# Performance work log

Measured on AMD Instinct MI355X. Metric: run time of the kernel, lower is better.

## Reference

```python
import jax, jax.numpy as jnp
import numpy as np

# TT factorization for fc1: 768 = 4*4*6*8 -> 3072 = 4*6*8*16, ranks (1,12,24,12,1)
# TT factorization for fc2: 3072 = 4*6*8*16 -> 768 = 4*4*6*8, ranks (1,12,24,12,1)
IN_F1, OUT_F1 = (4, 4, 6, 8), (4, 6, 8, 16)
IN_F2, OUT_F2 = (4, 6, 8, 16), (4, 4, 6, 8)
RANKS = (12, 24, 12)


def _core(key, shape, fan_in):
    return jax.random.normal(key, shape, dtype=jnp.float32) * (fan_in ** -0.5)


def make_tt_params(key, in_f, out_f, ranks):
    r = (1,) + tuple(ranks) + (1,)
    ks = jax.random.split(key, 5)
    # boundary cores squeeze the unit rank dims
    g1 = _core(ks[0], (in_f[0], out_f[0], r[1]), in_f[0])              # (i1,o1,r1)
    g2 = _core(ks[1], (r[1], in_f[1], out_f[1], r[2]), r[1] * in_f[1])  # (r1,i2,o2,r2)
    g3 = _core(ks[2], (r[2], in_f[2], out_f[2], r[3]), r[2] * in_f[2])  # (r2,i3,o3,r3)
    g4 = _core(ks[3], (r[3], in_f[3], out_f[3]), r[3] * in_f[3])        # (r3,i4,o4)
    b = jnp.zeros((int(np.prod(out_f)),), dtype=jnp.float32)
    return g1, g2, g3, g4, b


def tt_linear(x2d, g1, g2, g3, g4, bias, in_f):
    # x2d: (N, prod(in_f)) -> (N, prod(out_f))
    z = x2d.reshape((-1,) + tuple(in_f))                  # (b,i1,i2,i3,i4)
    z = jnp.einsum('bijkl,ipr->bjklpr', z, g1)            # (b,i2,i3,i4,o1,r1)
    z = jnp.einsum('bjklpr,rjqs->bklpqs', z, g2)          # (b,i3,i4,o1,o2,r2)
    z = jnp.einsum('bklpqs,sktu->blpqtu', z, g3)          # (b,i4,o1,o2,o3,r3)
    z = jnp.einsum('blpqtu,ulv->bpqtv', z, g4)            # (b,o1,o2,o3,o4)
    return z.reshape(z.shape[0], -1) + bias


def setup_inputs() -> dict:
    key = jax.random.key(0)
    kx, k1, k2 = jax.random.split(key, 3)
    x = jax.random.normal(kx, (2, 2048, 768), dtype=jnp.float32)
    g1a, g1b, g1c, g1d, b1 = make_tt_params(k1, IN_F1, OUT_F1, RANKS)
    g2a, g2b, g2c, g2d, b2 = make_tt_params(k2, IN_F2, OUT_F2, RANKS)
    return {"x": x, "g1a": g1a, "g1b": g1b, "g1c": g1c, "g1d": g1d, "b1": b1,
            "g2a": g2a, "g2b": g2b, "g2c": g2c, "g2d": g2d, "b2": b2}


def reference(x, g1a, g1b, g1c, g1d, b1, g2a, g2b, g2c, g2d, b2):
    B, S, D = x.shape
    h = tt_linear(x.reshape(-1, D), g1a, g1b, g1c, g1d, b1, IN_F1)  # (N, 3072)
    h = jax.nn.gelu(h, approximate=False)  # nn.GELU() default = exact erf
    # dropout: identity in eval mode
    y = tt_linear(h, g2a, g2b, g2c, g2d, b2, IN_F2)                 # (N, 768)
    return y.reshape(B, S, -1)
```

## Files before the change

kernel.cpp:

```cpp
#include <hip/hip_runtime.h>
#include <cstdint>
#include <cstddef>

typedef unsigned short u16;
typedef __attribute__((ext_vector_type(8))) __bf16 bf16x8;
typedef __attribute__((ext_vector_type(4))) float f32x4;

__device__ __forceinline__ u16 f2bf(float f) {
  unsigned u = __float_as_uint(f);
  u += 0x7FFFu + ((u >> 16) & 1u);
  return (u16)(u >> 16);
}

__device__ __forceinline__ float bf2f(u16 h) {
  return __uint_as_float(((unsigned)h) << 16);
}

__device__ __forceinline__ void async16(u16* lds, const u16* g) {
  __builtin_amdgcn_global_load_lds(
      (const __attribute__((address_space(1))) unsigned int*)g,
      (__attribute__((address_space(3))) unsigned int*)lds, 16, 0, 0);
}

__global__ __launch_bounds__(256)
void prep(const float4* __restrict__ x4, ushort4* __restrict__ xb4,
          const float* __restrict__ gA1, const float* __restrict__ gB1,
          const float* __restrict__ gC1, const float* __restrict__ gD1,
          const float* __restrict__ gA2, const float* __restrict__ gB2,
          const float* __restrict__ gC2, const float* __restrict__ gD2,
          float* __restrict__ B12_1, float* __restrict__ B12_2,
          float* __restrict__ C1, float* __restrict__ C2) {
  const int b = blockIdx.x;
  const int tid = threadIdx.x;
  if (b < 3072) {
    int i = b * 256 + tid;
    float4 v = x4[i];
    ushort4 o;
    o.x = f2bf(v.x); o.y = f2bf(v.y); o.z = f2bf(v.z); o.w = f2bf(v.w);
    xb4[i] = o;
    return;
  }
  int idx = (b - 3072) * 256 + tid;
  if (idx < 9216) {
    int e = idx;
    int r2 = e % 24; int t = e / 24;
    int fo12 = t % 24, fi12 = t / 24;
    int i2 = fi12 % 4, i1 = fi12 / 4;
    int o2 = fo12 % 6, o1 = fo12 / 6;
    float s = 0.f;
#pragma unroll
    for (int r1 = 0; r1 < 12; ++r1)
      s += gA1[(i1 * 4 + o1) * 12 + r1] * gB1[((r1 * 4 + i2) * 6 + o2) * 24 + r2];
    B12_1[e] = s;
  } else if (idx < 18432) {
    int e = idx - 9216;
    int r2 = e % 24; int t = e / 24;
    int fo12 = t % 16, fi12 = t / 16;
    int i2 = fi12 % 6, i1 = fi12 / 6;
    int o2 = fo12 % 4, o1 = fo12 / 4;
    float s = 0.f;
#pragma unroll
    for (int r1 = 0; r1 < 12; ++r1)
      s += gA2[(i1 * 4 + o1) * 12 + r1] * gB2[((r1 * 6 + i2) * 4 + o2) * 24 + r2];
    B12_2[e] = s;
  } else if (idx < 165888) {
    int e = idx - 18432;
    int fi34 = e % 48; int t = e / 48;
    int fo34 = t % 128;
    int i3 = fi34 / 8, i4 = fi34 % 8;
    int o3 = fo34 / 16, o4 = fo34 % 16;
    int r2 = t / 128;
    float s = 0.f;
#pragma unroll
    for (int r3 = 0; r3 < 12; ++r3)
      s += gC1[((r2 * 6 + i3) * 8 + o3) * 12 + r3] * gD1[(r3 * 8 + i4) * 16 + o4];
    C1[e] = s;
  } else {
    int e = idx - 165888;
    int fi34 = e % 128; int t = e / 128;
    int fo34 = t % 48;
    int i3 = fi34 / 16, i4 = fi34 % 16;
    int o3 = fo34 / 8, o4 = fo34 % 8;
    int r2 = t / 48;
    float s = 0.f;
#pragma unroll
    for (int r3 = 0; r3 < 12; ++r3)
      s += gC2[((r2 * 8 + i3) * 6 + o3) * 12 + r3] * gD2[(r3 * 16 + i4) * 8 + o4];
    C2[e] = s;
  }
}

template <int FI12, int I34, int O12, int O34, int OG>
__device__ __forceinline__
void tt_expand_body(const float* __restrict__ B12, const float* __restrict__ C34t,
                    u16* __restrict__ Wt, int bx, int by, int tid, float* sB) {
  constexpr int R2 = 24;
  constexpr int Kin = FI12 * I34;
  constexpr int IC = Kin / 8;
  constexpr int I34C = I34 / 8;
  for (int e = tid; e < FI12 * OG * R2; e += 256) {
    int r2 = e % R2; int t = e / R2;
    int f = t % OG; int fi12 = t / OG;
    sB[(fi12 * OG + f) * 25 + r2] = B12[(fi12 * O12 + by * OG + f) * R2 + r2];
  }
  __syncthreads();
  const int t = bx * 256 + tid;
  const int fo34 = t / IC;
  const int ic = t % IC;
  const int fi12 = ic / I34C;
  const int fi34 = (ic % I34C) * 8;

  float acc[OG][8];
#pragma unroll
  for (int f = 0; f < OG; ++f)
#pragma unroll
    for (int k = 0; k < 8; ++k) acc[f][k] = 0.f;

  for (int r2 = 0; r2 < R2; ++r2) {
    const float4* cp = (const float4*)(C34t + ((size_t)(r2 * O34 + fo34) * I34 + fi34));
    float4 c0 = cp[0], c1 = cp[1];
    float c[8] = {c0.x, c0.y, c0.z, c0.w, c1.x, c1.y, c1.z, c1.w};
#pragma unroll
    for (int f = 0; f < OG; ++f) {
      float bb = sB[(fi12 * OG + f) * 25 + r2];
#pragma unroll
      for (int k = 0; k < 8; ++k) acc[f][k] += bb * c[k];
    }
  }
#pragma unroll
  for (int f = 0; f < OG; ++f) {
    int out = (by * OG + f) * O34 + fo34;
    u16 v[8];
#pragma unroll
    for (int k = 0; k < 8; ++k) v[k] = f2bf(acc[f][k]);
    *(uint4*)(Wt + (size_t)out * Kin + fi12 * I34 + fi34) = *(const uint4*)v;
  }
}

__global__ __launch_bounds__(256)
void tt_expand2(const float* __restrict__ B12_1, const float* __restrict__ C1, u16* __restrict__ W1t,
                const float* __restrict__ B12_2, const float* __restrict__ C2, u16* __restrict__ W2t) {
  __shared__ float sB[24 * 4 * 25];
  const int b = blockIdx.x;
  const int tid = threadIdx.x;
  if (b < 288) {
    tt_expand_body<16, 48, 24, 128, 4>(B12_1, C1, W1t, b % 48, b / 48, tid, sB);
  } else {
    int bb = b - 288;
    tt_expand_body<24, 128, 16, 48, 4>(B12_2, C2, W2t, bb % 72, bb / 72, tid, sB);
  }
}

__global__ void reduceN8(const uint4* __restrict__ P, const float* __restrict__ bias,
                         float4* __restrict__ out4, int n8, int zstride8, int nz) {
  int i = blockIdx.x * 256 + threadIdx.x;
  if (i >= n8) return;
  int b0 = (i % 96) * 8;
  float a[8];
#pragma unroll
  for (int k = 0; k < 8; ++k) a[k] = bias[b0 + k];
  for (int s = 0; s < nz; ++s) {
    uint4 u = P[i + s * zstride8];
    const u16* up = (const u16*)&u;
#pragma unroll
    for (int k = 0; k < 8; ++k) a[k] += bf2f(up[k]);
  }
  out4[i * 2]     = (float4){a[0], a[1], a[2], a[3]};
  out4[i * 2 + 1] = (float4){a[4], a[5], a[6], a[7]};
}

template <bool GELU, int MAP>
__global__ __launch_bounds__(512, 2)
void gemm_bt(const u16* __restrict__ A, const u16* __restrict__ Bt,
             const float* __restrict__ bias, u16* __restrict__ Out,
             int N, int lda, int ldb, size_t zstride) {
  constexpr int NT = 12;
  const int flat = blockIdx.x;
  const int xcd = flat & 7;
  const int local = flat >> 3;
  int bm, bn, bz;
  if (MAP == 1) {
    bm = (xcd >> 1) * 4 + (local & 3);
    bn = (xcd & 1) * 8 + (local >> 2);
    bz = 0;
  } else {
    bz = xcd >> 1;
    bm = (xcd & 1) * 8 + (local & 7);
    bn = local >> 3;
  }
  const int kbeg = (MAP == 2) ? bz * 768 : 0;

  __shared__ __align__(16) u16 AL[2][16384];
  __shared__ __align__(16) u16 BL[3][12288];

  const int tid = threadIdx.x;
  const int wave = tid >> 6, lane = tid & 63;
  const int lr = lane & 15, lq = lane >> 4;
  const int wr = (wave >> 2) * 128;
  const int wc = (wave & 3) * 48;

  const int prow = tid >> 3;
  const int pcc  = (tid & 7) ^ (((tid >> 5) & 1) << 1);
  const u16* Ag = A + (size_t)(bm * 256 + prow) * lda + kbeg + pcc * 8;
  const u16* Bg = Bt + (size_t)(bn * 192 + prow) * ldb + kbeg + pcc * 8;

  auto stA = [&](int slot, int p, int k) {
    async16(&AL[slot][0] + p * 4096 + tid * 8, Ag + (size_t)(p * 64) * lda + k);
  };
  auto stB = [&](int slot, int p, int k) {
    async16(&BL[slot][0] + p * 4096 + tid * 8, Bg + (size_t)(p * 64) * ldb + k);
  };

  int aOff[2][8], bOff[2][3];
#pragma unroll
  for (int kk = 0; kk < 2; ++kk) {
#pragma unroll
    for (int mi = 0; mi < 8; ++mi) {
      int L = (wr + mi * 16 + lr) * 128 + kk * 64 + lq * 16;
      L ^= ((L >> 9) & 1) << 5;
      aOff[kk][mi] = L >> 1;
    }
#pragma unroll
    for (int nj = 0; nj < 3; ++nj) {
      int L = (wc + nj * 16 + lr) * 128 + kk * 64 + lq * 16;
      L ^= ((L >> 9) & 1) << 5;
      bOff[kk][nj] = L >> 1;
    }
  }

  f32x4 acc[8][3];
#pragma unroll
  for (int mi = 0; mi < 8; ++mi)
#pragma unroll
    for (int nj = 0; nj < 3; ++nj) acc[mi][nj] = (f32x4){0.f, 0.f, 0.f, 0.f};

  stA(0, 0, 0); stA(0, 1, 0); stA(0, 2, 0); stA(0, 3, 0);
  stB(0, 0, 0); stB(0, 1, 0); stB(0, 2, 0);
  stB(1, 0, 64); stB(1, 1, 64); stB(1, 2, 64);
  asm volatile("s_waitcnt vmcnt(3)" ::: "memory");
  __builtin_amdgcn_s_barrier();
  __builtin_amdgcn_sched_barrier(0);

  int bsR = 0, bsW = 2;
  for (int t = 0; t < NT; ++t) {
    const u16* Ab = &AL[t & 1][0];
    const u16* Bb = &BL[bsR][0];
    const int wAs = (t + 1) & 1;
    const int kA = ((t + 1 < NT) ? t + 1 : NT - 1) * 64;
    const int kB = ((t + 2 < NT) ? t + 2 : NT - 1) * 64;

    bf16x8 bf[3], af[4], af2[4];
#pragma unroll
    for (int nj = 0; nj < 3; ++nj) bf[nj] = *(const bf16x8*)(Bb + bOff[0][nj]);
#pragma unroll
    for (int mi = 0; mi < 4; ++mi) af[mi] = *(const bf16x8*)(Ab + aOff[0][mi]);
    stA(wAs, 0, kA); stA(wAs, 1, kA);
    __builtin_amdgcn_s_barrier();
    asm volatile("s_waitcnt lgkmcnt(0)" ::: "memory");
    __builtin_amdgcn_sched_barrier(0);
    __builtin_amdgcn_s_setprio(1);
#pragma unroll
    for (int mi = 0; mi < 4; ++mi)
#pragma unroll
      for (int nj = 0; nj < 3; ++nj)
        acc[mi][nj] = __builtin_amdgcn_mfma_f32_16x16x32_bf16(af[mi], bf[nj], acc[mi][nj], 0, 0, 0);
    __builtin_amdgcn_s_setprio(0);
    __builtin_amdgcn_s_barrier();
    __builtin_amdgcn_sched_barrier(0);
#pragma unroll
    for (int mi = 0; mi < 4; ++mi) af2[mi] = *(const bf16x8*)(Ab + aOff[0][4 + mi]);
    stA(wAs, 2, kA); stA(wAs, 3, kA);
    __builtin_amdgcn_s_barrier();
    asm volatile("s_waitcnt lgkmcnt(0)" ::: "memory");
    __builtin_amdgcn_sched_barrier(0);
    __builtin_amdgcn_s_setprio(1);
#pragma unroll
    for (int mi = 0; mi < 4; ++mi)
#pragma unroll
      for (int nj = 0; nj < 3; ++nj)
        acc[4 + mi][nj] = __builtin_amdgcn_mfma_f32_16x16x32_bf16(af2[mi], bf[nj], acc[4 + mi][nj], 0, 0, 0);
    __builtin_amdgcn_s_setprio(0);
    __builtin_amdgcn_s_barrier();
    __builtin_amdgcn_sched_barrier(0);
#pragma unroll
    for (int nj = 0; nj < 3; ++nj) bf[nj] = *(const bf16x8*)(Bb + bOff[1][nj]);
#pragma unroll
    for (int mi = 0; mi < 4; ++mi) af[mi] = *(const bf16x8*)(Ab + aOff[1][mi]);
    stB(bsW, 0, kB); stB(bsW, 1, kB);
    __builtin_amdgcn_s_barrier();
    asm volatile("s_waitcnt lgkmcnt(0)" ::: "memory");
    __builtin_amdgcn_sched_barrier(0);
    __builtin_amdgcn_s_setprio(1);
#pragma unroll
    for (int mi = 0; mi < 4; ++mi)
#pragma unroll
      for (int nj = 0; nj < 3; ++nj)
        acc[mi][nj] = __builtin_amdgcn_mfma_f32_16x16x32_bf16(af[mi], bf[nj], acc[mi][nj], 0, 0, 0);
    __builtin_amdgcn_s_setprio(0);
    __builtin_amdgcn_s_barrier();
    __builtin_amdgcn_sched_barrier(0);
#pragma unroll
    for (int mi = 0; mi < 4; ++mi) af2[mi] = *(const bf16x8*)(Ab + aOff[1][4 + mi]);
    stB(bsW, 2, kB);
    __builtin_amdgcn_s_barrier();
    asm volatile("s_waitcnt lgkmcnt(0)" ::: "memory");
    __builtin_amdgcn_sched_barrier(0);
    __builtin_amdgcn_s_setprio(1);
#pragma unroll
    for (int mi = 0; mi < 4; ++mi)
#pragma unroll
      for (int nj = 0; nj < 3; ++nj)
        acc[4 + mi][nj] = __builtin_amdgcn_mfma_f32_16x16x32_bf16(af2[mi], bf[nj], acc[4 + mi][nj], 0, 0, 0);
    __builtin_amdgcn_s_setprio(0);
    asm volatile("s_waitcnt vmcnt(3)" ::: "memory");
    __builtin_amdgcn_s_barrier();
    __builtin_amdgcn_sched_barrier(0);

    bsR = (bsR + 1 == 3) ? 0 : bsR + 1;
    bsW = (bsW + 1 == 3) ? 0 : bsW + 1;
  }

  u16* Op = Out + (size_t)bz * zstride;
  const int r0 = bm * 256 + wr + lq * 4;
  const int c0 = bn * 192 + wc + lr;
  float bv[3];
  if (GELU) {
#pragma unroll
    for (int nj = 0; nj < 3; ++nj) bv[nj] = bias[c0 + nj * 16];
  }
#pragma unroll
  for (int mi = 0; mi < 8; ++mi) {
#pragma unroll
    for (int r = 0; r < 4; ++r) {
      const size_t rowoff = (size_t)(r0 + mi * 16 + r) * N;
#pragma unroll
      for (int nj = 0; nj < 3; ++nj) {
        float v = acc[mi][nj][r];
        if (GELU) {
          v += bv[nj];
          float inner = v * fmaf(v * v, 0.0356774081f, 0.7978845608f);
          float e = __builtin_amdgcn_exp2f(2.8853900818f * inner);
          float r1 = __builtin_amdgcn_rcpf(1.0f + e);
          v = v - v * r1;
        }
        Op[rowoff + c0 + nj * 16] = f2bf(v);
      }
    }
  }
}

extern "C" void kernel_launch(void* const* d_in, const int* in_sizes, int n_in,
                              void* d_out, int out_size, void* d_ws, size_t ws_size,
                              hipStream_t stream) {
  const float* x   = (const float*)d_in[0];
  const float* g1a = (const float*)d_in[1];
  const float* g1b = (const float*)d_in[2];
  const float* g1c = (const float*)d_in[3];
  const float* g1d = (const float*)d_in[4];
  const float* b1  = (const float*)d_in[5];
  const float* g2a = (const float*)d_in[6];
  const float* g2b = (const float*)d_in[7];
  const float* g2c = (const float*)d_in[8];
  const float* g2d = (const float*)d_in[9];
  const float* b2  = (const float*)d_in[10];
  float* out = (float*)d_out;

  char* ws = (char*)d_ws;
  u16* xb   = (u16*)(ws + 0);
  u16* W1t  = (u16*)(ws + 6291456);
  u16* W2t  = (u16*)(ws + 11010048);
  u16* h    = (u16*)(ws + 15728640);
  u16* Part = (u16*)(ws + 40894464);
  float* B12_1 = (float*)(ws + 40894464);
  float* B12_2 = (float*)(ws + 40894464 + 36864);
  float* C1    = (float*)(ws + 40894464 + 73728);
  float* C2    = (float*)(ws + 40894464 + 663552);

  prep<<<4296, 256, 0, stream>>>((const float4*)x, (ushort4*)xb,
                                 g1a, g1b, g1c, g1d, g2a, g2b, g2c, g2d,
                                 B12_1, B12_2, C1, C2);

  tt_expand2<<<576, 256, 0, stream>>>(B12_1, C1, W1t, B12_2, C2, W2t);

  gemm_bt<true, 1><<<256, 512, 0, stream>>>(xb, W1t, b1, h, 3072, 768, 768, 0);
  gemm_bt<false, 2><<<256, 512, 0, stream>>>(h, W2t, nullptr, Part, 768, 3072, 3072, 3145728);
  reduceN8<<<1536, 256, 0, stream>>>((const uint4*)Part, b2,
                                     (float4*)out, 393216, 393216, 4);
}
```

Measured before the change: 160.1 us.

## Shrink GEMM tiles to 128x96 with 4 waves and halve split-K

Reworks the bf16 GEMM kernel to use 128x96 output tiles with 256 threads (4 waves, each 64x48) in place of 256x192 tiles with 512 threads. This quadruples the block count for fc1 and doubles it for fc2, so the per-iteration pipeline drops from four MFMA phases to two. For fc2 the split-K factor goes from 4 to 2 with 24 K-steps per block, which halves the partial buffers the reduction reads. The aim is better occupancy and less partial-sum traffic, at the cost of lower operand reuse per tile and more global and LDS traffic per FLOP.

```diff
diff --git a/kernel.cpp b/kernel.cpp
--- a/kernel.cpp
+++ b/kernel.cpp
@@ -169,68 +169,67 @@
   out4[i * 2 + 1] = (float4){a[4], a[5], a[6], a[7]};
 }
 
-template <bool GELU, int MAP>
-__global__ __launch_bounds__(512, 2)
+template <bool GELU, int MAP, int NT>
+__global__ __launch_bounds__(256, 2)
 void gemm_bt(const u16* __restrict__ A, const u16* __restrict__ Bt,
              const float* __restrict__ bias, u16* __restrict__ Out,
              int N, int lda, int ldb, size_t zstride) {
-  constexpr int NT = 12;
   const int flat = blockIdx.x;
   const int xcd = flat & 7;
   const int local = flat >> 3;
   int bm, bn, bz;
   if (MAP == 1) {
-    bm = (xcd >> 1) * 4 + (local & 3);
-    bn = (xcd & 1) * 8 + (local >> 2);
+    bm = (xcd >> 1) * 8 + (local & 7);
+    bn = (xcd & 1) * 16 + (local >> 3);
     bz = 0;
   } else {
-    bz = xcd >> 1;
-    bm = (xcd & 1) * 8 + (local & 7);
+    bz = xcd & 1;
+    bm = (xcd >> 1) * 8 + (local & 7);
     bn = local >> 3;
   }
-  const int kbeg = (MAP == 2) ? bz * 768 : 0;
-
-  __shared__ __align__(16) u16 AL[2][16384];
-  __shared__ __align__(16) u16 BL[3][12288];
+  const int kbeg = (MAP == 2) ? bz * 1536 : 0;
+
+  __shared__ __align__(16) u16 AL[2][8192];
+  __shared__ __align__(16) u16 BL[3][6144];
 
   const int tid = threadIdx.x;
   const int wave = tid >> 6, lane = tid & 63;
   const int lr = lane & 15, lq = lane >> 4;
-  const int wr = (wave >> 2) * 128;
-  const int wc = (wave & 3) * 48;
+  const int wm = (wave & 1) * 64;
+  const int wn = (wave >> 1) * 48;
 
   const int prow = tid >> 3;
   const int pcc  = (tid & 7) ^ (((tid >> 5) & 1) << 1);
-  const u16* Ag = A + (size_t)(bm * 256 + prow) * lda + kbeg + pcc * 8;
-  const u16* Bg = Bt + (size_t)(bn * 192 + prow) * ldb + kbeg + pcc * 8;
+  const u16* Ag = A + (size_t)(bm * 128 + prow) * lda + kbeg + pcc * 8;
+  const u16* Bg = Bt + (size_t)(bn * 96 + prow) * ldb + kbeg + pcc * 8;
 
   auto stA = [&](int slot, int p, int k) {
-    async16(&AL[slot][0] + p * 4096 + tid * 8, Ag + (size_t)(p * 64) * lda + k);
+    async16(&AL[slot][0] + p * 2048 + tid * 8, Ag + (size_t)(p * 32) * lda + k);
   };
   auto stB = [&](int slot, int p, int k) {
-    async16(&BL[slot][0] + p * 4096 + tid * 8, Bg + (size_t)(p * 64) * ldb + k);
+    async16(&BL[slot][0] + p * 2048 + tid * 8, Bg + (size_t)(p * 32) * ldb + k);
   };
 
-  int aOff[2][8], bOff[2][3];
+  int aOff[2][4], bOff[2][3];
 #pragma unroll
   for (int kk = 0; kk < 2; ++kk) {
 #pragma unroll
-    for (int mi = 0; mi < 8; ++mi) {
-      int L = (wr + mi * 16 + lr) * 128 + kk * 64 + lq * 16;
+    for (int mi = 0; mi < 4; ++mi) {
+      int L = (wm + mi * 16 + lr) * 128 + kk * 64 + lq * 16;
       L ^= ((L >> 9) & 1) << 5;
       aOff[kk][mi] = L >> 1;
     }
 #pragma unroll
     for (int nj = 0; nj < 3; ++nj) {
-      int L = (wc + nj * 16 + lr) * 128 + kk * 64 + lq * 16;
+      int L = (wn + nj * 16 + lr) * 128 + kk * 64 + lq * 16;
       L ^= ((L >> 9) & 1) << 5;
       bOff[kk][nj] = L >> 1;
     }
   }
 
-  f32x4 acc[8][3];
-#pragma unroll
-  for (int mi = 0; mi < 8; ++mi)
+  f32x4 acc[4][3];
+#pragma unroll
+  for (int mi = 0; mi < 4; ++mi)
 #pragma unroll
     for (int nj = 0; nj < 3; ++nj) acc[mi][nj] = (f32x4){0.f, 0.f, 0.f, 0.f};
 
@@ -249,12 +248,12 @@
     const int kA = ((t + 1 < NT) ? t + 1 : NT - 1) * 64;
     const int kB = ((t + 2 < NT) ? t + 2 : NT - 1) * 64;
 
-    bf16x8 bf[3], af[4], af2[4];
+    bf16x8 bf[3], af[4];
 #pragma unroll
     for (int nj = 0; nj < 3; ++nj) bf[nj] = *(const bf16x8*)(Bb + bOff[0][nj]);
 #pragma unroll
     for (int mi = 0; mi < 4; ++mi) af[mi] = *(const bf16x8*)(Ab + aOff[0][mi]);
-    stA(wAs, 0, kA); stA(wAs, 1, kA);
+    stA(wAs, 0, kA); stA(wAs, 1, kA); stA(wAs, 2, kA); stA(wAs, 3, kA);
     __builtin_amdgcn_s_barrier();
     asm volatile("s_waitcnt lgkmcnt(0)" ::: "memory");
     __builtin_amdgcn_sched_barrier(0);
@@ -268,8 +267,10 @@
     __builtin_amdgcn_s_barrier();
     __builtin_amdgcn_sched_barrier(0);
 #pragma unroll
-    for (int mi = 0; mi < 4; ++mi) af2[mi] = *(const bf16x8*)(Ab + aOff[0][4 + mi]);
-    stA(wAs, 2, kA); stA(wAs, 3, kA);
+    for (int nj = 0; nj < 3; ++nj) bf[nj] = *(const bf16x8*)(Bb + bOff[1][nj]);
+#pragma unroll
+    for (int mi = 0; mi < 4; ++mi) af[mi] = *(const bf16x8*)(Ab + aOff[1][mi]);
+    stB(bsW, 0, kB); stB(bsW, 1, kB); stB(bsW, 2, kB);
     __builtin_amdgcn_s_barrier();
     asm volatile("s_waitcnt lgkmcnt(0)" ::: "memory");
     __builtin_amdgcn_sched_barrier(0);
@@ -278,39 +279,7 @@
     for (int mi = 0; mi < 4; ++mi)
 #pragma unroll
       for (int nj = 0; nj < 3; ++nj)
-        acc[4 + mi][nj] = __builtin_amdgcn_mfma_f32_16x16x32_bf16(af2[mi], bf[nj], acc[4 + mi][nj], 0, 0, 0);
-    __builtin_amdgcn_s_setprio(0);
-    __builtin_amdgcn_s_barrier();
-    __builtin_amdgcn_sched_barrier(0);
-#pragma unroll
-    for (int nj = 0; nj < 3; ++nj) bf[nj] = *(const bf16x8*)(Bb + bOff[1][nj]);
-#pragma unroll
-    for (int mi = 0; mi < 4; ++mi) af[mi] = *(const bf16x8*)(Ab + aOff[1][mi]);
-    stB(bsW, 0, kB); stB(bsW, 1, kB);
-    __builtin_amdgcn_s_barrier();
-    asm volatile("s_waitcnt lgkmcnt(0)" ::: "memory");
-    __builtin_amdgcn_sched_barrier(0);
-    __builtin_amdgcn_s_setprio(1);
-#pragma unroll
-    for (int mi = 0; mi < 4; ++mi)
-#pragma unroll
-      for (int nj = 0; nj < 3; ++nj)
         acc[mi][nj] = __builtin_amdgcn_mfma_f32_16x16x32_bf16(af[mi], bf[nj], acc[mi][nj], 0, 0, 0);
-    __builtin_amdgcn_s_setprio(0);
-    __builtin_amdgcn_s_barrier();
-    __builtin_amdgcn_sched_barrier(0);
-#pragma unroll
-    for (int mi = 0; mi < 4; ++mi) af2[mi] = *(const bf16x8*)(Ab + aOff[1][4 + mi]);
-    stB(bsW, 2, kB);
-    __builtin_amdgcn_s_barrier();
-    asm volatile("s_waitcnt lgkmcnt(0)" ::: "memory");
-    __builtin_amdgcn_sched_barrier(0);
-    __builtin_amdgcn_s_setprio(1);
-#pragma unroll
-    for (int mi = 0; mi < 4; ++mi)
-#pragma unroll
-      for (int nj = 0; nj < 3; ++nj)
-        acc[4 + mi][nj] = __builtin_amdgcn_mfma_f32_16x16x32_bf16(af2[mi], bf[nj], acc[4 + mi][nj], 0, 0, 0);
     __builtin_amdgcn_s_setprio(0);
     asm volatile("s_waitcnt vmcnt(3)" ::: "memory");
     __builtin_amdgcn_s_barrier();
@@ -321,15 +290,15 @@
   }
 
   u16* Op = Out + (size_t)bz * zstride;
-  const int r0 = bm * 256 + wr + lq * 4;
-  const int c0 = bn * 192 + wc + lr;
+  const int r0 = bm * 128 + wm + lq * 4;
+  const int c0 = bn * 96 + wn + lr;
   float bv[3];
   if (GELU) {
 #pragma unroll
     for (int nj = 0; nj < 3; ++nj) bv[nj] = bias[c0 + nj * 16];
   }
 #pragma unroll
-  for (int mi = 0; mi < 8; ++mi) {
+  for (int mi = 0; mi < 4; ++mi) {
 #pragma unroll
     for (int r = 0; r < 4; ++r) {
       const size_t rowoff = (size_t)(r0 + mi * 16 + r) * N;
@@ -382,8 +351,8 @@
 
   tt_expand2<<<576, 256, 0, stream>>>(B12_1, C1, W1t, B12_2, C2, W2t);
 
-  gemm_bt<true, 1><<<256, 512, 0, stream>>>(xb, W1t, b1, h, 3072, 768, 768, 0);
-  gemm_bt<false, 2><<<256, 512, 0, stream>>>(h, W2t, nullptr, Part, 768, 3072, 3072, 3145728);
+  gemm_bt<true, 1, 12><<<1024, 256, 0, stream>>>(xb, W1t, b1, h, 3072, 768, 768, 0);
+  gemm_bt<false, 2, 24><<<512, 256, 0, stream>>>(h, W2t, nullptr, Part, 768, 3072, 3072, 3145728);
   reduceN8<<<1536, 256, 0, stream>>>((const uint4*)Part, b2,
-                                     (float4*)out, 393216, 393216, 4);
-}
+                                     (float4*)out, 393216, 393216, 2);
+}
```

Measured after the change: 156.9 us, median of 2. -2.0%, faster.
